# Optimization experiments

Hardware: AMD Instinct MI355X
Metric: run time of the kernel (lower is better)

## Reference

```python
import jax, jax.numpy as jnp
import numpy as np

N = 100000
NEG_SLOPE = 0.2


def gat_conv(x, edge_index, W, att_src, att_dst, bias, heads, out_ch, concat):
    # x: [N, F_in]; W: [F_in, heads*out_ch]; att_*: [heads, out_ch]; bias per PyG
    h = (x @ W).reshape(N, heads, out_ch)  # [N, H, C]
    # add self loops (PyG default add_self_loops=True)
    loop = jnp.arange(N, dtype=edge_index.dtype)
    src = jnp.concatenate([edge_index[0], loop])  # [E+N]
    dst = jnp.concatenate([edge_index[1], loop])
    a_src = jnp.einsum('nhc,hc->nh', h, att_src)  # [N, H]
    a_dst = jnp.einsum('nhc,hc->nh', h, att_dst)
    e = jax.nn.leaky_relu(a_src[src] + a_dst[dst], NEG_SLOPE)  # [E+N, H]
    # segment softmax over destination nodes (numerically stable)
    m = jax.ops.segment_max(e, dst, num_segments=N)
    e = jnp.exp(e - m[dst])
    denom = jax.ops.segment_sum(e, dst, num_segments=N)
    alpha = e / (denom[dst] + 1e-16)  # [E+N, H]
    # weighted scatter-add aggregation
    out = jax.ops.segment_sum(h[src] * alpha[:, :, None], dst, num_segments=N)  # [N,H,C]
    if concat:
        out = out.reshape(N, heads * out_ch)
    else:
        out = out.mean(axis=1)
    return out + bias


def setup_inputs() -> dict:
    key = jax.random.key(0)
    ks = jax.random.split(key, 10)
    F_in, H1, C1, NCLS = 512, 8, 8, 40
    E = 1600000
    x = jax.random.normal(ks[0], (N, F_in), dtype=jnp.float32)
    edge_index = jax.random.randint(ks[1], (2, E), 0, N, dtype=jnp.int64)
    s1 = 1.0 / np.sqrt(F_in)
    s2 = 1.0 / np.sqrt(H1 * C1)
    return {
        'x': x,
        'edge_index': edge_index,
        'W1': jax.random.normal(ks[2], (F_in, H1 * C1), dtype=jnp.float32) * s1,
        'att_src1': jax.random.normal(ks[3], (H1, C1), dtype=jnp.float32) * 0.1,
        'att_dst1': jax.random.normal(ks[4], (H1, C1), dtype=jnp.float32) * 0.1,
        'b1': jnp.zeros((H1 * C1,), dtype=jnp.float32),
        'W2': jax.random.normal(ks[5], (H1 * C1, NCLS), dtype=jnp.float32) * s2,
        'att_src2': jax.random.normal(ks[6], (1, NCLS), dtype=jnp.float32) * 0.1,
        'att_dst2': jax.random.normal(ks[7], (1, NCLS), dtype=jnp.float32) * 0.1,
        'b2': jnp.zeros((NCLS,), dtype=jnp.float32),
    }


def reference(x, edge_index, W1, att_src1, att_dst1, b1, W2, att_src2, att_dst2, b2):
    # dropout in eval mode -> identity
    h = gat_conv(x, edge_index, W1, att_src1, att_dst1, b1, heads=8, out_ch=8, concat=True)
    h = jax.nn.elu(h)
    NCLS = W2.shape[1]
    out = gat_conv(h, edge_index, W2, att_src2, att_dst2, b2, heads=1, out_ch=NCLS, concat=False)
    return jax.nn.softmax(out, axis=1)
```

## Files before the change

kernel.cpp:

```cpp
#include <hip/hip_runtime.h>
#include <math.h>

#define N_NODES 100000
#define FIN     512
#define H1H     8
#define C1C     8
#define HC1     64
#define NCLS    40
#define NEG_SLOPE 0.2f

#define NPB   256
#define NBUK  391
#define EPB   4096

#define TM 128
#define TN 64
#define BK 16
#define XS_LD 132

__global__ __launch_bounds__(256) void k_gemm1(const float* __restrict__ x,
                                               const float* __restrict__ W1,
                                               float* __restrict__ h1) {
    __shared__ float xs[2][BK][XS_LD];
    __shared__ float ws[2][BK][TN];
    const int tx = threadIdx.x;
    const int row_base = blockIdx.x * TM;
    const int cg = (tx & 15) << 2;
    const int rg = (tx >> 4) << 3;

    float4 xr4[2];
    float4 wr4;

    auto load_regs = [&](int k0) {
#pragma unroll
        for (int i = 0; i < 2; i++) {
            const int f  = tx + 256 * i;
            const int r  = f >> 2;
            const int kq = (f & 3) << 2;
            const int gr = row_base + r;
            xr4[i] = (gr < N_NODES) ? *(const float4*)(x + (size_t)gr * FIN + k0 + kq)
                                    : make_float4(0.f, 0.f, 0.f, 0.f);
        }
        {
            const int kk = tx >> 4;
            const int c4 = (tx & 15) << 2;
            wr4 = *(const float4*)(W1 + (size_t)(k0 + kk) * TN + c4);
        }
    };
    auto store_lds = [&](int buf) {
#pragma unroll
        for (int i = 0; i < 2; i++) {
            const int f  = tx + 256 * i;
            const int r  = f >> 2;
            const int kq = (f & 3) << 2;
            xs[buf][kq + 0][r] = xr4[i].x;
            xs[buf][kq + 1][r] = xr4[i].y;
            xs[buf][kq + 2][r] = xr4[i].z;
            xs[buf][kq + 3][r] = xr4[i].w;
        }
        {
            const int kk = tx >> 4;
            const int c4 = (tx & 15) << 2;
            *(float4*)&ws[buf][kk][c4] = wr4;
        }
    };

    float acc[8][4];
#pragma unroll
    for (int i = 0; i < 8; i++)
#pragma unroll
        for (int j = 0; j < 4; j++) acc[i][j] = 0.f;

    load_regs(0);
    store_lds(0);
    __syncthreads();

    int buf = 0;
    for (int k0 = 0; k0 < FIN; k0 += BK, buf ^= 1) {
        const bool more = (k0 + BK < FIN);
        if (more) load_regs(k0 + BK);
#pragma unroll
        for (int k = 0; k < BK; k++) {
            const float4 xa = *(const float4*)&xs[buf][k][rg];
            const float4 xb = *(const float4*)&xs[buf][k][rg + 4];
            const float4 wv = *(const float4*)&ws[buf][k][cg];
            const float xr[8] = {xa.x, xa.y, xa.z, xa.w, xb.x, xb.y, xb.z, xb.w};
#pragma unroll
            for (int i = 0; i < 8; i++) {
                acc[i][0] = fmaf(xr[i], wv.x, acc[i][0]);
                acc[i][1] = fmaf(xr[i], wv.y, acc[i][1]);
                acc[i][2] = fmaf(xr[i], wv.z, acc[i][2]);
                acc[i][3] = fmaf(xr[i], wv.w, acc[i][3]);
            }
        }
        if (more) {
            store_lds(buf ^ 1);
            __syncthreads();
        }
    }
#pragma unroll
    for (int i = 0; i < 8; i++) {
        const int gr = row_base + rg + i;
        if (gr < N_NODES)
            *(float4*)(h1 + (size_t)gr * HC1 + cg) =
                make_float4(acc[i][0], acc[i][1], acc[i][2], acc[i][3]);
    }
}

__global__ __launch_bounds__(256) void k_att1(const float* __restrict__ h1,
                                              const float* __restrict__ att_src,
                                              const float* __restrict__ att_dst,
                                              float* __restrict__ a_src,
                                              float* __restrict__ a_dst) {
    const int tid = blockIdx.x * 256 + threadIdx.x;
    if (tid >= N_NODES * H1H) return;
    const int n = tid >> 3, hh = tid & 7;
    const float* hp = h1 + (size_t)n * HC1 + hh * C1C;
    float s = 0.f, d = 0.f;
#pragma unroll
    for (int c = 0; c < C1C; c++) {
        const float v = hp[c];
        s = fmaf(v, att_src[hh * C1C + c], s);
        d = fmaf(v, att_dst[hh * C1C + c], d);
    }
    a_src[tid] = s;
    a_dst[tid] = d;
}

__global__ __launch_bounds__(256) void k_bcnt(const int* __restrict__ dst, int E,
                                              int* __restrict__ gcnt) {
    __shared__ int lcnt[NBUK];
    for (int i = threadIdx.x; i < NBUK; i += 256) lcnt[i] = 0;
    __syncthreads();
    const int e0 = blockIdx.x * EPB;
#pragma unroll
    for (int i = 0; i < EPB / 256; i++) {
        const int e = e0 + i * 256 + threadIdx.x;
        if (e < E) atomicAdd(&lcnt[dst[e] >> 8], 1);
    }
    __syncthreads();
    for (int i = threadIdx.x; i < NBUK; i += 256)
        if (lcnt[i]) atomicAdd(&gcnt[i], lcnt[i]);
}

__global__ __launch_bounds__(512) void k_bscan(const int* __restrict__ gcnt,
                                               int* __restrict__ gbase,
                                               int* __restrict__ gcur, int E) {
    __shared__ int sm[512];
    const int t = threadIdx.x;
    const int v = (t < NBUK) ? gcnt[t] : 0;
    sm[t] = v;
    __syncthreads();
    for (int off = 1; off < 512; off <<= 1) {
        const int u = (t >= off) ? sm[t - off] : 0;
        __syncthreads();
        sm[t] += u;
        __syncthreads();
    }
    if (t < NBUK) {
        const int b = sm[t] - v;
        gbase[t] = b;
        gcur[t]  = b;
    }
    if (t == 0) gbase[NBUK] = E;
}

__global__ __launch_bounds__(256) void k_bfill(const int* __restrict__ src,
                                               const int* __restrict__ dst, int E,
                                               int* __restrict__ gcur,
                                               int2* __restrict__ pairs) {
    __shared__ int lcnt[NBUK];
    __shared__ int lbase[NBUK];
    for (int i = threadIdx.x; i < NBUK; i += 256) lcnt[i] = 0;
    __syncthreads();
    const int e0 = blockIdx.x * EPB;
#pragma unroll
    for (int i = 0; i < EPB / 256; i++) {
        const int e = e0 + i * 256 + threadIdx.x;
        if (e < E) atomicAdd(&lcnt[dst[e] >> 8], 1);
    }
    __syncthreads();
    for (int i = threadIdx.x; i < NBUK; i += 256)
        lbase[i] = lcnt[i] ? atomicAdd(&gcur[i], lcnt[i]) : 0;
    __syncthreads();
#pragma unroll
    for (int i = 0; i < EPB / 256; i++) {
        const int e = e0 + i * 256 + threadIdx.x;
        if (e < E) {
            const int d = dst[e];
            const int pos = atomicAdd(&lbase[d >> 8], 1);
            pairs[pos] = make_int2(src[e], d);
        }
    }
}

__global__ __launch_bounds__(256) void k_bscatter(const int2* __restrict__ pairs,
                                                  const int* __restrict__ gbase,
                                                  int* __restrict__ offs,
                                                  int* __restrict__ srcsort, int E) {
    __shared__ int ldeg[NPB];
    __shared__ int ltmp[NPB];
    __shared__ int lcur[NPB];
    const int b = blockIdx.x;
    const int tx = threadIdx.x;
    const int node0 = b << 8;
    const int pbeg = gbase[b];
    const int cnt  = gbase[b + 1] - pbeg;

    ldeg[tx] = 0;
    __syncthreads();
    for (int i = tx; i < cnt; i += 256)
        atomicAdd(&ldeg[pairs[pbeg + i].y - node0], 1);
    __syncthreads();
    const int v = ldeg[tx];
    ltmp[tx] = v;
    __syncthreads();
    for (int off = 1; off < 256; off <<= 1) {
        const int u = (tx >= off) ? ltmp[tx - off] : 0;
        __syncthreads();
        ltmp[tx] += u;
        __syncthreads();
    }
    const int mypos = pbeg + ltmp[tx] - v;
    if (node0 + tx < N_NODES) offs[node0 + tx] = mypos;
    lcur[tx] = mypos;
    if (b == NBUK - 1 && tx == 0) offs[N_NODES] = E;
    __syncthreads();
    for (int i = tx; i < cnt; i += 256) {
        const int2 p = pairs[pbeg + i];
        const int pos = atomicAdd(&lcur[p.y - node0], 1);
        srcsort[pos] = p.x;
    }
}

__global__ __launch_bounds__(256) void k_agg1(const float* __restrict__ h1,
                                              const float* __restrict__ a_src,
                                              const float* __restrict__ a_dst,
                                              const int* __restrict__ offs,
                                              const int* __restrict__ srcsort,
                                              const float* __restrict__ b1,
                                              float* __restrict__ h1e) {
    const int n = blockIdx.x * 4 + (threadIdx.x >> 6);
    if (n >= N_NODES) return;
    const int lane = threadIdx.x & 63;
    const int hh   = lane >> 3;
    const float adn = a_dst[n * H1H + hh];
    const int beg = offs[n], end = offs[n + 1];

    float e0 = a_src[n * H1H + hh] + adn;
    e0 = e0 > 0.f ? e0 : NEG_SLOPE * e0;
    float m = e0;
    float denom = 1.f;
    float acc = h1[(size_t)n * HC1 + lane];

    int j = beg;
    for (; j + 4 <= end; j += 4) {
        const int s0 = srcsort[j], s1 = srcsort[j + 1];
        const int s2 = srcsort[j + 2], s3 = srcsort[j + 3];
        const float q0 = a_src[s0 * H1H + hh], q1 = a_src[s1 * H1H + hh];
        const float q2 = a_src[s2 * H1H + hh], q3 = a_src[s3 * H1H + hh];
        const float g0 = h1[(size_t)s0 * HC1 + lane];
        const float g1 = h1[(size_t)s1 * HC1 + lane];
        const float g2 = h1[(size_t)s2 * HC1 + lane];
        const float g3 = h1[(size_t)s3 * HC1 + lane];
        float f0 = q0 + adn; f0 = f0 > 0.f ? f0 : NEG_SLOPE * f0;
        float f1 = q1 + adn; f1 = f1 > 0.f ? f1 : NEG_SLOPE * f1;
        float f2 = q2 + adn; f2 = f2 > 0.f ? f2 : NEG_SLOPE * f2;
        float f3 = q3 + adn; f3 = f3 > 0.f ? f3 : NEG_SLOPE * f3;
        const float nm = fmaxf(m, fmaxf(fmaxf(f0, f1), fmaxf(f2, f3)));
        const float sc = __expf(m - nm);
        const float w0 = __expf(f0 - nm), w1 = __expf(f1 - nm);
        const float w2 = __expf(f2 - nm), w3 = __expf(f3 - nm);
        denom = fmaf(denom, sc, (w0 + w1) + (w2 + w3));
        acc = fmaf(acc, sc, fmaf(w0, g0, fmaf(w1, g1, fmaf(w2, g2, w3 * g3))));
        m = nm;
    }
    for (; j < end; j++) {
        const int s = srcsort[j];
        float e = a_src[s * H1H + hh] + adn;
        e = e > 0.f ? e : NEG_SLOPE * e;
        const float g = h1[(size_t)s * HC1 + lane];
        const float nm = fmaxf(m, e);
        const float sc = __expf(m - nm);
        const float w = __expf(e - nm);
        denom = fmaf(denom, sc, w);
        acc = fmaf(acc, sc, w * g);
        m = nm;
    }
    float v = acc / denom + b1[lane];
    h1e[(size_t)n * HC1 + lane] = v > 0.f ? v : (__expf(v) - 1.f);
}

__global__ __launch_bounds__(256) void k_gemm2(const float* __restrict__ h1e,
                                               const float* __restrict__ W2,
                                               const float* __restrict__ att_src2,
                                               const float* __restrict__ att_dst2,
                                               float* __restrict__ h2,
                                               float* __restrict__ a_src2,
                                               float* __restrict__ a_dst2) {
    const int n = blockIdx.x * 4 + (threadIdx.x >> 6);
    if (n >= N_NODES) return;
    const int lane = threadIdx.x & 63;
    const float xv = h1e[(size_t)n * HC1 + lane];
    float acc = 0.f;
#pragma unroll
    for (int k = 0; k < HC1; k++) {
        const float xk = __shfl(xv, k, 64);
        const float wv = (lane < NCLS) ? W2[k * NCLS + lane] : 0.f;
        acc = fmaf(xk, wv, acc);
    }
    if (lane < NCLS) h2[(size_t)n * NCLS + lane] = acc;
    float ps = (lane < NCLS) ? acc * att_src2[lane] : 0.f;
    float pd = (lane < NCLS) ? acc * att_dst2[lane] : 0.f;
#pragma unroll
    for (int off = 32; off; off >>= 1) {
        ps += __shfl_xor(ps, off, 64);
        pd += __shfl_xor(pd, off, 64);
    }
    if (lane == 0) {
        a_src2[n] = ps;
        a_dst2[n] = pd;
    }
}

__global__ __launch_bounds__(256) void k_agg2(const float* __restrict__ h2,
                                              const float* __restrict__ a_src,
                                              const float* __restrict__ a_dst,
                                              const int* __restrict__ offs,
                                              const int* __restrict__ srcsort,
                                              const float* __restrict__ b2,
                                              float* __restrict__ out) {
    const int n = blockIdx.x * 4 + (threadIdx.x >> 6);
    if (n >= N_NODES) return;
    const int lane = threadIdx.x & 63;
    const float adn = a_dst[n];
    const int beg = offs[n], end = offs[n + 1];

    float e0 = a_src[n] + adn;
    e0 = e0 > 0.f ? e0 : NEG_SLOPE * e0;
    float m = e0;
    float denom = 1.f;
    float acc = (lane < NCLS) ? h2[(size_t)n * NCLS + lane] : 0.f;

    int j = beg;
    for (; j + 4 <= end; j += 4) {
        const int s0 = srcsort[j], s1 = srcsort[j + 1];
        const int s2 = srcsort[j + 2], s3 = srcsort[j + 3];
        const float q0 = a_src[s0], q1 = a_src[s1];
        const float q2 = a_src[s2], q3 = a_src[s3];
        float g0 = 0.f, g1 = 0.f, g2 = 0.f, g3 = 0.f;
        if (lane < NCLS) {
            g0 = h2[(size_t)s0 * NCLS + lane];
            g1 = h2[(size_t)s1 * NCLS + lane];
            g2 = h2[(size_t)s2 * NCLS + lane];
            g3 = h2[(size_t)s3 * NCLS + lane];
        }
        float f0 = q0 + adn; f0 = f0 > 0.f ? f0 : NEG_SLOPE * f0;
        float f1 = q1 + adn; f1 = f1 > 0.f ? f1 : NEG_SLOPE * f1;
        float f2 = q2 + adn; f2 = f2 > 0.f ? f2 : NEG_SLOPE * f2;
        float f3 = q3 + adn; f3 = f3 > 0.f ? f3 : NEG_SLOPE * f3;
        const float nm = fmaxf(m, fmaxf(fmaxf(f0, f1), fmaxf(f2, f3)));
        const float sc = __expf(m - nm);
        const float w0 = __expf(f0 - nm), w1 = __expf(f1 - nm);
        const float w2 = __expf(f2 - nm), w3 = __expf(f3 - nm);
        denom = fmaf(denom, sc, (w0 + w1) + (w2 + w3));
        acc = fmaf(acc, sc, fmaf(w0, g0, fmaf(w1, g1, fmaf(w2, g2, w3 * g3))));
        m = nm;
    }
    for (; j < end; j++) {
        const int s = srcsort[j];
        float e = a_src[s] + adn;
        e = e > 0.f ? e : NEG_SLOPE * e;
        const float g = (lane < NCLS) ? h2[(size_t)s * NCLS + lane] : 0.f;
        const float nm = fmaxf(m, e);
        const float sc = __expf(m - nm);
        const float w = __expf(e - nm);
        denom = fmaf(denom, sc, w);
        acc = fmaf(acc, sc, w * g);
        m = nm;
    }
    float o = (lane < NCLS) ? (acc / denom + b2[lane]) : -INFINITY;
    float mx = o;
#pragma unroll
    for (int off = 32; off; off >>= 1) mx = fmaxf(mx, __shfl_xor(mx, off, 64));
    const float ex = (lane < NCLS) ? __expf(o - mx) : 0.f;
    float sm = ex;
#pragma unroll
    for (int off = 32; off; off >>= 1) sm += __shfl_xor(sm, off, 64);
    if (lane < NCLS) out[(size_t)n * NCLS + lane] = ex / sm;
}

extern "C" void kernel_launch(void* const* d_in, const int* in_sizes, int n_in,
                              void* d_out, int out_size, void* d_ws, size_t ws_size,
                              hipStream_t stream) {
    const float* x   = (const float*)d_in[0];
    const int*   ei  = (const int*)d_in[1];
    const float* W1v = (const float*)d_in[2];
    const float* as1 = (const float*)d_in[3];
    const float* ad1 = (const float*)d_in[4];
    const float* b1  = (const float*)d_in[5];
    const float* W2v = (const float*)d_in[6];
    const float* as2 = (const float*)d_in[7];
    const float* ad2 = (const float*)d_in[8];
    const float* b2  = (const float*)d_in[9];
    const int E = in_sizes[1] / 2;
    const int* esrc = ei;
    const int* edst = ei + E;

    char* wp = (char*)d_ws;
    auto alloc = [&](size_t bytes) {
        char* p = wp;
        wp += (bytes + 255) & ~(size_t)255;
        return p;
    };
    float* h1     = (float*)alloc((size_t)N_NODES * HC1 * 4);
    float* h1e    = (float*)alloc((size_t)N_NODES * HC1 * 4);
    float* a_src1 = (float*)alloc((size_t)N_NODES * H1H * 4);
    float* a_dst1 = (float*)alloc((size_t)N_NODES * H1H * 4);
    float* a_src2 = (float*)alloc((size_t)N_NODES * 4);
    float* a_dst2 = (float*)alloc((size_t)N_NODES * 4);
    int*   offs   = (int*)alloc((size_t)(N_NODES + 1) * 4);
    int*   gcnt   = (int*)alloc((size_t)NBUK * 4);
    int*   gbase  = (int*)alloc((size_t)(NBUK + 1) * 4);
    int*   gcur   = (int*)alloc((size_t)NBUK * 4);
    int*   srcsort= (int*)alloc((size_t)E * 4);
    int2*  pairs  = (int2*)alloc((size_t)E * 8);
    float* h2     = h1;

    hipMemsetAsync(gcnt, 0, (size_t)NBUK * 4, stream);

    const int NEB = (E + EPB - 1) / EPB;
    k_gemm1<<<(N_NODES + TM - 1) / TM, 256, 0, stream>>>(x, W1v, h1);
    k_att1<<<(N_NODES * H1H + 255) / 256, 256, 0, stream>>>(h1, as1, ad1, a_src1, a_dst1);
    k_bcnt<<<NEB, 256, 0, stream>>>(edst, E, gcnt);
    k_bscan<<<1, 512, 0, stream>>>(gcnt, gbase, gcur, E);
    k_bfill<<<NEB, 256, 0, stream>>>(esrc, edst, E, gcur, pairs);
    k_bscatter<<<NBUK, 256, 0, stream>>>(pairs, gbase, offs, srcsort, E);
    k_agg1<<<(N_NODES + 3) / 4, 256, 0, stream>>>(h1, a_src1, a_dst1, offs, srcsort, b1, h1e);
    k_gemm2<<<(N_NODES + 3) / 4, 256, 0, stream>>>(h1e, W2v, as2, ad2, h2, a_src2, a_dst2);
    k_agg2<<<(N_NODES + 3) / 4, 256, 0, stream>>>(h2, a_src2, a_dst2, offs, srcsort, b2, (float*)d_out);
}
```

Baseline: 696.3 us.

## Fuse attention logits into GEMM1 epilogue and tile GEMM2 through shared memory

The separate k_att1 kernel is removed. Per-head source and destination attention logits are now computed in the GEMM1 epilogue from register accumulators, with one lane shuffle to combine the two 4-column halves of each head. GEMM2 is rewritten from a one-wavefront-per-node shuffle loop into a 128-node tiled kernel. That kernel stages h1e and a transposed W2 in shared memory and computes 4 nodes by 5 classes per thread, then reduces the attention logits across 8 lanes. This removes one launch and a re-read of h1, and cuts GEMM2's redundant global W2 loads. In exchange it adds more shared memory use and uncoalesced 5-wide h2 stores.

```diff
diff --git a/kernel.cpp b/kernel.cpp
--- a/kernel.cpp
+++ b/kernel.cpp
@@ -20,7 +20,11 @@
 
 __global__ __launch_bounds__(256) void k_gemm1(const float* __restrict__ x,
                                                const float* __restrict__ W1,
-                                               float* __restrict__ h1) {
+                                               const float* __restrict__ att_src,
+                                               const float* __restrict__ att_dst,
+                                               float* __restrict__ h1,
+                                               float* __restrict__ a_src,
+                                               float* __restrict__ a_dst) {
     __shared__ float xs[2][BK][XS_LD];
     __shared__ float ws[2][BK][TN];
     const int tx = threadIdx.x;
@@ -98,33 +102,25 @@
             __syncthreads();
         }
     }
+
+    const float4 asv = *(const float4*)(att_src + cg);
+    const float4 adv = *(const float4*)(att_dst + cg);
+    const int head = cg >> 3;
 #pragma unroll
     for (int i = 0; i < 8; i++) {
         const int gr = row_base + rg + i;
         if (gr < N_NODES)
             *(float4*)(h1 + (size_t)gr * HC1 + cg) =
                 make_float4(acc[i][0], acc[i][1], acc[i][2], acc[i][3]);
-    }
-}
-
-__global__ __launch_bounds__(256) void k_att1(const float* __restrict__ h1,
-                                              const float* __restrict__ att_src,
-                                              const float* __restrict__ att_dst,
-                                              float* __restrict__ a_src,
-                                              float* __restrict__ a_dst) {
-    const int tid = blockIdx.x * 256 + threadIdx.x;
-    if (tid >= N_NODES * H1H) return;
-    const int n = tid >> 3, hh = tid & 7;
-    const float* hp = h1 + (size_t)n * HC1 + hh * C1C;
-    float s = 0.f, d = 0.f;
-#pragma unroll
-    for (int c = 0; c < C1C; c++) {
-        const float v = hp[c];
-        s = fmaf(v, att_src[hh * C1C + c], s);
-        d = fmaf(v, att_dst[hh * C1C + c], d);
-    }
-    a_src[tid] = s;
-    a_dst[tid] = d;
+        float ps = acc[i][0] * asv.x + acc[i][1] * asv.y + acc[i][2] * asv.z + acc[i][3] * asv.w;
+        float pd = acc[i][0] * adv.x + acc[i][1] * adv.y + acc[i][2] * adv.z + acc[i][3] * adv.w;
+        ps += __shfl_xor(ps, 1, 64);
+        pd += __shfl_xor(pd, 1, 64);
+        if (!(tx & 1) && gr < N_NODES) {
+            a_src[gr * H1H + head] = ps;
+            a_dst[gr * H1H + head] = pd;
+        }
+    }
 }
 
 __global__ __launch_bounds__(256) void k_bcnt(const int* __restrict__ dst, int E,
@@ -291,6 +287,7 @@
     h1e[(size_t)n * HC1 + lane] = v > 0.f ? v : (__expf(v) - 1.f);
 }
 
+#define TM2 128
 __global__ __launch_bounds__(256) void k_gemm2(const float* __restrict__ h1e,
                                                const float* __restrict__ W2,
                                                const float* __restrict__ att_src2,
@@ -298,28 +295,95 @@
                                                float* __restrict__ h2,
                                                float* __restrict__ a_src2,
                                                float* __restrict__ a_dst2) {
-    const int n = blockIdx.x * 4 + (threadIdx.x >> 6);
-    if (n >= N_NODES) return;
-    const int lane = threadIdx.x & 63;
-    const float xv = h1e[(size_t)n * HC1 + lane];
-    float acc = 0.f;
-#pragma unroll
-    for (int k = 0; k < HC1; k++) {
-        const float xk = __shfl(xv, k, 64);
-        const float wv = (lane < NCLS) ? W2[k * NCLS + lane] : 0.f;
-        acc = fmaf(xk, wv, acc);
-    }
-    if (lane < NCLS) h2[(size_t)n * NCLS + lane] = acc;
-    float ps = (lane < NCLS) ? acc * att_src2[lane] : 0.f;
-    float pd = (lane < NCLS) ? acc * att_dst2[lane] : 0.f;
-#pragma unroll
-    for (int off = 32; off; off >>= 1) {
-        ps += __shfl_xor(ps, off, 64);
-        pd += __shfl_xor(pd, off, 64);
-    }
-    if (lane == 0) {
-        a_src2[n] = ps;
-        a_dst2[n] = pd;
+    __shared__ float hs[32][65][4];
+    __shared__ float w2t[NCLS][68];
+    __shared__ float asv[NCLS], adv[NCLS];
+    const int tx = threadIdx.x;
+    const int node0 = blockIdx.x * TM2;
+
+    for (int f = tx; f < HC1 * NCLS; f += 256) {
+        const int k = f / NCLS, c = f - k * NCLS;
+        w2t[c][k] = W2[f];
+    }
+    if (tx < NCLS) {
+        asv[tx] = att_src2[tx];
+        adv[tx] = att_dst2[tx];
+    }
+#pragma unroll
+    for (int i = 0; i < 8; i++) {
+        const int f  = tx + 256 * i;
+        const int n  = f >> 4;
+        const int k4 = (f & 15) << 2;
+        const int gn = node0 + n;
+        const float4 v = (gn < N_NODES) ? *(const float4*)(h1e + (size_t)gn * HC1 + k4)
+                                        : make_float4(0.f, 0.f, 0.f, 0.f);
+        const int ng = n >> 2, ni = n & 3;
+        hs[ng][k4 + 0][ni] = v.x;
+        hs[ng][k4 + 1][ni] = v.y;
+        hs[ng][k4 + 2][ni] = v.z;
+        hs[ng][k4 + 3][ni] = v.w;
+    }
+    __syncthreads();
+
+    const int ng = tx >> 3;
+    const int cg = tx & 7;
+    const int c0 = cg * 5;
+
+    float acc[4][5];
+#pragma unroll
+    for (int i = 0; i < 4; i++)
+#pragma unroll
+        for (int j = 0; j < 5; j++) acc[i][j] = 0.f;
+
+    for (int k = 0; k < HC1; k += 4) {
+        float4 hv[4];
+#pragma unroll
+        for (int t = 0; t < 4; t++) hv[t] = *(const float4*)&hs[ng][k + t][0];
+#pragma unroll
+        for (int j = 0; j < 5; j++) {
+            const float4 wv = *(const float4*)&w2t[c0 + j][k];
+            acc[0][j] = fmaf(hv[0].x, wv.x, fmaf(hv[1].x, wv.y, fmaf(hv[2].x, wv.z, fmaf(hv[3].x, wv.w, acc[0][j]))));
+            acc[1][j] = fmaf(hv[0].y, wv.x, fmaf(hv[1].y, wv.y, fmaf(hv[2].y, wv.z, fmaf(hv[3].y, wv.w, acc[1][j]))));
+            acc[2][j] = fmaf(hv[0].z, wv.x, fmaf(hv[1].z, wv.y, fmaf(hv[2].z, wv.z, fmaf(hv[3].z, wv.w, acc[2][j]))));
+            acc[3][j] = fmaf(hv[0].w, wv.x, fmaf(hv[1].w, wv.y, fmaf(hv[2].w, wv.z, fmaf(hv[3].w, wv.w, acc[3][j]))));
+        }
+    }
+
+    float ps[4], pd[4];
+#pragma unroll
+    for (int i = 0; i < 4; i++) {
+        const int gn = node0 + ng * 4 + i;
+        float s = 0.f, d = 0.f;
+#pragma unroll
+        for (int j = 0; j < 5; j++) {
+            s = fmaf(acc[i][j], asv[c0 + j], s);
+            d = fmaf(acc[i][j], adv[c0 + j], d);
+        }
+        ps[i] = s;
+        pd[i] = d;
+        if (gn < N_NODES) {
+#pragma unroll
+            for (int j = 0; j < 5; j++)
+                h2[(size_t)gn * NCLS + c0 + j] = acc[i][j];
+        }
+    }
+#pragma unroll
+    for (int off = 1; off < 8; off <<= 1) {
+#pragma unroll
+        for (int i = 0; i < 4; i++) {
+            ps[i] += __shfl_xor(ps[i], off, 64);
+            pd[i] += __shfl_xor(pd[i], off, 64);
+        }
+    }
+    if (cg == 0) {
+#pragma unroll
+        for (int i = 0; i < 4; i++) {
+            const int gn = node0 + ng * 4 + i;
+            if (gn < N_NODES) {
+                a_src2[gn] = ps[i];
+                a_dst2[gn] = pd[i];
+            }
+        }
     }
 }
 
@@ -430,13 +494,12 @@
     hipMemsetAsync(gcnt, 0, (size_t)NBUK * 4, stream);
 
     const int NEB = (E + EPB - 1) / EPB;
-    k_gemm1<<<(N_NODES + TM - 1) / TM, 256, 0, stream>>>(x, W1v, h1);
-    k_att1<<<(N_NODES * H1H + 255) / 256, 256, 0, stream>>>(h1, as1, ad1, a_src1, a_dst1);
+    k_gemm1<<<(N_NODES + TM - 1) / TM, 256, 0, stream>>>(x, W1v, as1, ad1, h1, a_src1, a_dst1);
     k_bcnt<<<NEB, 256, 0, stream>>>(edst, E, gcnt);
     k_bscan<<<1, 512, 0, stream>>>(gcnt, gbase, gcur, E);
     k_bfill<<<NEB, 256, 0, stream>>>(esrc, edst, E, gcur, pairs);
     k_bscatter<<<NBUK, 256, 0, stream>>>(pairs, gbase, offs, srcsort, E);
     k_agg1<<<(N_NODES + 3) / 4, 256, 0, stream>>>(h1, a_src1, a_dst1, offs, srcsort, b1, h1e);
-    k_gemm2<<<(N_NODES + 3) / 4, 256, 0, stream>>>(h1e, W2v, as2, ad2, h2, a_src2, a_dst2);
+    k_gemm2<<<(N_NODES + TM2 - 1) / TM2, 256, 0, stream>>>(h1e, W2v, as2, ad2, h2, a_src2, a_dst2);
     k_agg2<<<(N_NODES + 3) / 4, 256, 0, stream>>>(h2, a_src2, a_dst2, offs, srcsort, b2, (float*)d_out);
 }
```

Measured after the change: 609.4 us. 1.14x faster.
